# Optimization experiments

Measured on AMD Instinct MI355X. Metric: run time of the kernel, lower is better.

Reference implementation:

```python
import jax, jax.numpy as jnp
import numpy as np
import math

B, T, D, H, P, NPASS = 2, 2048, 1024, 16, 256, 3


def setup_inputs() -> dict:
    key = jax.random.key(0)
    ks = jax.random.split(key, 8)
    x = jax.random.normal(ks[0], (B, T, D), jnp.float32)
    scale_gamma = 1.0 + 0.1 * jax.random.normal(ks[1], (D,), jnp.float32)
    scale_beta = 0.1 * jax.random.normal(ks[2], (D,), jnp.float32)
    qkv_w = 0.02 * jax.random.normal(ks[3], (3 * D, D), jnp.float32)
    o_w = 0.02 * jax.random.normal(ks[4], (D, D), jnp.float32)
    norm1_w = jnp.ones((D,), jnp.float32)
    norm2_w = jnp.ones((D,), jnp.float32)
    angles = 0.1 * jax.random.normal(ks[5], (NPASS, P), jnp.float32)
    gate = jnp.ones((NPASS, D), jnp.float32)
    bias = jnp.zeros((NPASS, D), jnp.float32)
    # seeded random permutations matching torch.manual_seed(42+p*1000); torch.randperm
    pis, pjs = [], []
    for p in range(NPASS):
        rng = np.random.RandomState(42 + p * 1000)
        perm = rng.permutation(D)
        pis.append(perm[:P])
        pjs.append(perm[P:2 * P])
    pi = jnp.asarray(np.stack(pis), jnp.int32)
    pj = jnp.asarray(np.stack(pjs), jnp.int32)
    return dict(x=x, scale_gamma=scale_gamma, scale_beta=scale_beta, qkv_w=qkv_w,
                o_w=o_w, norm1_w=norm1_w, norm2_w=norm2_w, angles=angles,
                gate=gate, bias=bias, pi=pi, pj=pj)


def _rmsnorm(x, w):
    eps = jnp.finfo(x.dtype).eps
    return x * jax.lax.rsqrt(jnp.mean(x * x, axis=-1, keepdims=True) + eps) * w


def reference(x, scale_gamma, scale_beta, qkv_w, o_w, norm1_w, norm2_w,
              angles, gate, bias, pi, pj):
    Bs, Ts, Ds = x.shape
    hd = Ds // H
    # --- attention branch ---
    h = _rmsnorm(x, norm1_w) * scale_gamma + scale_beta
    qkv = (h @ qkv_w.T).reshape(Bs, Ts, 3, H, hd)
    qkv = jnp.moveaxis(qkv, 2, 0)            # [3, B, T, H, hd]
    q, k, v = (jnp.swapaxes(qkv[i], 1, 2) for i in range(3))  # [B, H, T, hd]
    scores = jnp.einsum('bhqd,bhkd->bhqk', q, k) / math.sqrt(hd)
    causal = jnp.tril(jnp.ones((Ts, Ts), bool))
    scores = jnp.where(causal, scores, -jnp.inf)
    attn = jax.nn.softmax(scores, axis=-1)
    out = jnp.einsum('bhqk,bhkd->bhqd', attn, v)
    out = jnp.swapaxes(out, 1, 2).reshape(Bs, Ts, Ds)
    x = x + out @ o_w.T
    # --- rotation pseudo-FFN branch ---
    h = _rmsnorm(x, norm2_w) * scale_gamma + scale_beta
    r = h
    for p in range(NPASS):
        cos_a = jnp.cos(angles[p])
        sin_a = jnp.sin(angles[p])
        hi = r[..., pi[p]]
        hj = r[..., pj[p]]
        r = r.at[..., pi[p]].set(hi * cos_a - hj * sin_a)
        r = r.at[..., pj[p]].set(hi * sin_a + hj * cos_a)
        r = jax.nn.silu(r * gate[p] + bias[p])
    return x + r - h
```

## Files before the change

kernel.cpp:

```cpp
#include <hip/hip_runtime.h>
#include <hip/hip_bf16.h>

#define B_ 2
#define T_ 2048
#define D_ 1024
#define H_ 16
#define HD_ 64
#define NP_ 3
#define P_ 256

#define SCALE2 0.18033688011112042f

typedef short bf16x8 __attribute__((ext_vector_type(8)));
typedef float f32x4 __attribute__((ext_vector_type(4)));

__device__ __forceinline__ float bf2f(__hip_bfloat16 v) { return __bfloat162float(v); }
__device__ __forceinline__ __hip_bfloat16 f2bf(float v) { return __float2bfloat16(v); }

__device__ __forceinline__ unsigned pack2bf(float a, float b) {
    unsigned r;
    asm("v_cvt_pk_bf16_f32 %0, %1, %2" : "=v"(r) : "v"(a), "v"(b));
    return r;
}
__device__ __forceinline__ unsigned short f2bf_u(float v) {
    return (unsigned short)pack2bf(v, v);
}

#define GLOAD_LDS16(gp, lp) \
    __builtin_amdgcn_global_load_lds( \
        (const __attribute__((address_space(1))) void*)(gp), \
        (__attribute__((address_space(3))) void*)(lp), 16, 0, 0)

__global__ __launch_bounds__(256) void detect_kernel(
    const unsigned short* __restrict__ xs, int* __restrict__ flag)
{
    __shared__ int cnt;
    if (threadIdx.x == 0) cnt = 0;
    __syncthreads();
    int bad = 0;
    for (int i = threadIdx.x; i < 16384; i += 256) {
        int e = (xs[i] >> 7) & 0xFF;
        if (e >= 0xB8) bad++;
    }
    if (bad) atomicAdd(&cnt, bad);
    __syncthreads();
    if (threadIdx.x == 0) *flag = (cnt >= 8) ? 1 : 0;
}

__global__ __launch_bounds__(256) void cvt16_2_kernel(
    const void* __restrict__ a, const void* __restrict__ bsrc,
    __hip_bfloat16* __restrict__ da, __hip_bfloat16* __restrict__ db,
    int na, int ntot, const int* __restrict__ flag)
{
    int i8 = (blockIdx.x * 256 + threadIdx.x) * 8;
    if (i8 >= ntot) return;
    int f = *flag;
    const void* src; __hip_bfloat16* dst; int off;
    if (i8 < na) { src = a; dst = da; off = i8; }
    else         { src = bsrc; dst = db; off = i8 - na; }
    if (f) {
        const float4* sp = (const float4*)((const float*)src + off);
        float4 v0 = sp[0], v1 = sp[1];
        uint4 o;
        o.x = pack2bf(v0.x, v0.y);
        o.y = pack2bf(v0.z, v0.w);
        o.z = pack2bf(v1.x, v1.y);
        o.w = pack2bf(v1.z, v1.w);
        *(uint4*)(dst + off) = o;
    } else {
        *(uint4*)(dst + off) = *(const uint4*)((const __hip_bfloat16*)src + off);
    }
}

__global__ __launch_bounds__(256) void cvt_small_kernel(
    const void* __restrict__ g,  const void* __restrict__ b,
    const void* __restrict__ n1, const void* __restrict__ n2,
    const void* __restrict__ ang, const void* __restrict__ gt,
    const void* __restrict__ bi,
    float* __restrict__ dst, const int* __restrict__ flag)
{
    int i = blockIdx.x * 256 + threadIdx.x;
    if (i >= 11008) return;
    const void* src; int off;
    if      (i < 1024) { src = g;   off = i; }
    else if (i < 2048) { src = b;   off = i - 1024; }
    else if (i < 3072) { src = n1;  off = i - 2048; }
    else if (i < 4096) { src = n2;  off = i - 3072; }
    else if (i < 4864) { src = ang; off = i - 4096; }
    else if (i < 7936) { src = gt;  off = i - 4864; }
    else               { src = bi;  off = i - 7936; }
    dst[i] = (*flag) ? ((const float*)src)[off]
                     : bf2f(((const __hip_bfloat16*)src)[off]);
}

__global__ __launch_bounds__(256) void rmsnorm1_kernel(
    const void* __restrict__ xraw,
    const float* __restrict__ gamma,
    const float* __restrict__ beta,
    const float* __restrict__ w,
    const int* __restrict__ flag,
    __hip_bfloat16* __restrict__ out)
{
    int row = blockIdx.x;
    int t = threadIdx.x;
    int f = *flag;
    float eps = f ? 1.1920929e-7f : 0.0078125f;
    float v[4];
    if (f) {
        const float4 xv = ((const float4*)((const float*)xraw + (size_t)row * D_))[t];
        v[0] = xv.x; v[1] = xv.y; v[2] = xv.z; v[3] = xv.w;
    } else {
        const uint2 u = ((const uint2*)((const __hip_bfloat16*)xraw + (size_t)row * D_))[t];
        v[0] = __uint_as_float(u.x << 16);
        v[1] = __uint_as_float(u.x & 0xffff0000u);
        v[2] = __uint_as_float(u.y << 16);
        v[3] = __uint_as_float(u.y & 0xffff0000u);
    }
    float ss = 0.f;
#pragma unroll
    for (int c = 0; c < 4; c++) ss += v[c] * v[c];
#pragma unroll
    for (int m = 32; m; m >>= 1) ss += __shfl_xor(ss, m, 64);
    __shared__ float red[4];
    int wv = t >> 6;
    if ((t & 63) == 0) red[wv] = ss;
    __syncthreads();
    float scale = rsqrtf((red[0] + red[1] + red[2] + red[3]) * (1.0f / D_) + eps);
    float o[4];
#pragma unroll
    for (int c = 0; c < 4; c++) {
        int e = t * 4 + c;
        o[c] = v[c] * scale * w[e] * gamma[e] + beta[e];
    }
    uint2 pkd;
    pkd.x = pack2bf(o[0], o[1]);
    pkd.y = pack2bf(o[2], o[3]);
    *(uint2*)(out + (size_t)row * D_ + t * 4) = pkd;
}

__global__ __launch_bounds__(256) void gemm_bt_bf16_kernel(
    const __hip_bfloat16* __restrict__ A,
    const __hip_bfloat16* __restrict__ Bm,
    __hip_bfloat16* __restrict__ C,
    int M, int N, int K, int nscale, float qscale)
{
    __shared__ __attribute__((aligned(16))) __hip_bfloat16 As[128 * 32];
    __shared__ __attribute__((aligned(16))) __hip_bfloat16 Bs[128 * 32];
    int tid = threadIdx.x;
    int bm = blockIdx.y, bn = blockIdx.x;
    int lane = tid & 63, wv = tid >> 6;
    int wm = wv >> 1, wn = wv & 1;
    int q = lane >> 4, mr = lane & 15;

    f32x4 acc[4][4] = {};

    for (int k0 = 0; k0 < K; k0 += 32) {
#pragma unroll
        for (int s = 0; s < 2; s++) {
            int e = (s * 256 + tid) * 8;
            int r = e >> 5, c = e & 31;
            GLOAD_LDS16(&A[(size_t)(bm * 128 + r) * K + k0 + c], &As[e]);
            GLOAD_LDS16(&Bm[(size_t)(bn * 128 + r) * K + k0 + c], &Bs[e]);
        }
        __syncthreads();
        bf16x8 af[4], bfr[4];
#pragma unroll
        for (int i = 0; i < 4; i++)
            af[i] = *(const bf16x8*)(&As[(wm * 64 + i * 16 + mr) * 32 + q * 8]);
#pragma unroll
        for (int j = 0; j < 4; j++)
            bfr[j] = *(const bf16x8*)(&Bs[(wn * 64 + j * 16 + mr) * 32 + q * 8]);
#pragma unroll
        for (int i = 0; i < 4; i++)
#pragma unroll
            for (int j = 0; j < 4; j++)
                acc[i][j] = __builtin_amdgcn_mfma_f32_16x16x32_bf16(af[i], bfr[j], acc[i][j], 0, 0, 0);
        __syncthreads();
    }

#pragma unroll
    for (int i = 0; i < 4; i++)
#pragma unroll
        for (int r = 0; r < 4; r++) {
            int m = bm * 128 + wm * 64 + i * 16 + q * 4 + r;
#pragma unroll
            for (int j = 0; j < 4; j++) {
                int n = bn * 128 + wn * 64 + j * 16 + mr;
                float vv = acc[i][j][r];
                if (n < nscale) vv *= qscale;
                ((unsigned short*)C)[(size_t)m * N + n] = f2bf_u(vv);
            }
        }
}

__global__ __launch_bounds__(256) void gemm_bt_resid_kernel(
    const __hip_bfloat16* __restrict__ A,
    const __hip_bfloat16* __restrict__ Bm,
    const void* __restrict__ xraw,
    const int* __restrict__ flag,
    float* __restrict__ C,
    int M, int N, int K)
{
    __shared__ __attribute__((aligned(16))) __hip_bfloat16 As[128 * 32];
    __shared__ __attribute__((aligned(16))) __hip_bfloat16 Bs[128 * 32];
    int tid = threadIdx.x;
    int bm = blockIdx.y, bn = blockIdx.x;
    int lane = tid & 63, wv = tid >> 6;
    int wm = wv >> 1, wn = wv & 1;
    int q = lane >> 4, mr = lane & 15;
    int f = *flag;

    f32x4 acc[4][4] = {};

    for (int k0 = 0; k0 < K; k0 += 32) {
#pragma unroll
        for (int s = 0; s < 2; s++) {
            int e = (s * 256 + tid) * 8;
            int r = e >> 5, c = e & 31;
            GLOAD_LDS16(&A[(size_t)(bm * 128 + r) * K + k0 + c], &As[e]);
            GLOAD_LDS16(&Bm[(size_t)(bn * 128 + r) * K + k0 + c], &Bs[e]);
        }
        __syncthreads();
        bf16x8 af[4], bfr[4];
#pragma unroll
        for (int i = 0; i < 4; i++)
            af[i] = *(const bf16x8*)(&As[(wm * 64 + i * 16 + mr) * 32 + q * 8]);
#pragma unroll
        for (int j = 0; j < 4; j++)
            bfr[j] = *(const bf16x8*)(&Bs[(wn * 64 + j * 16 + mr) * 32 + q * 8]);
#pragma unroll
        for (int i = 0; i < 4; i++)
#pragma unroll
            for (int j = 0; j < 4; j++)
                acc[i][j] = __builtin_amdgcn_mfma_f32_16x16x32_bf16(af[i], bfr[j], acc[i][j], 0, 0, 0);
        __syncthreads();
    }

#pragma unroll
    for (int i = 0; i < 4; i++)
#pragma unroll
        for (int r = 0; r < 4; r++) {
            int m = bm * 128 + wm * 64 + i * 16 + q * 4 + r;
#pragma unroll
            for (int j = 0; j < 4; j++) {
                int n = bn * 128 + wn * 64 + j * 16 + mr;
                size_t idx = (size_t)m * N + n;
                float rv = f ? ((const float*)xraw)[idx]
                             : bf2f(((const __hip_bfloat16*)xraw)[idx]);
                C[idx] = rv + acc[i][j][r];
            }
        }
}

__global__ __launch_bounds__(256, 4) void attn_kernel(
    const __hip_bfloat16* __restrict__ qkv,
    __hip_bfloat16* __restrict__ attn_out)
{
    __shared__ __attribute__((aligned(16))) __hip_bfloat16 Ks[2][64 * 64];
    __shared__ __attribute__((aligned(16))) __hip_bfloat16 Vts[2][64 * 64];
    __shared__ __attribute__((aligned(16))) unsigned int Pd[4 * 512];

    int id = blockIdx.x;
    int half = (id ^ (id >> 8)) & 1;
    int w4 = (id >> 1) & 15;
    int qt = half ? 31 - w4 : w4;
    int bh = (id >> 5) & 31;
    int b = bh >> 4, h = bh & 15;
    int tid = threadIdx.x, lane = tid & 63, wv = tid >> 6;
    int q = lane >> 4, mr = lane & 15;
    int m8 = mr & 7;

    const size_t rs3 = 3 * D_;
    const __hip_bfloat16* qp = qkv + (size_t)(b * T_) * rs3 + h * HD_;
    const __hip_bfloat16* kp = qp + D_;
    const __hip_bfloat16* vp = qp + 2 * D_;

    int sr = tid >> 2;
    int sc = (tid & 3) * 16;
    int lc0 = sc >> 3;
    int swk = sr & 7;
    int kk_ = (tid & 31) * 2;
    int dd = (tid >> 5) * 8;
    int vlc = kk_ >> 3, voff = kk_ & 7;

    bf16x8 aq0, aq1;
    {
        const __hip_bfloat16* qrow = qp + (size_t)(qt * 64 + wv * 16 + mr) * rs3;
        aq0 = *(const bf16x8*)(qrow + q * 8);
        aq1 = *(const bf16x8*)(qrow + 32 + q * 8);
    }

    bf16x8 kr0 = *(const bf16x8*)(kp + (size_t)sr * rs3 + sc);
    bf16x8 kr1 = *(const bf16x8*)(kp + (size_t)sr * rs3 + sc + 8);
    bf16x8 vr0 = *(const bf16x8*)(vp + (size_t)kk_ * rs3 + dd);
    bf16x8 vr1 = *(const bf16x8*)(vp + (size_t)(kk_ + 1) * rs3 + dd);
    *(bf16x8*)(&Ks[0][sr * 64 + ((lc0 ^ swk) * 8)]) = kr0;
    *(bf16x8*)(&Ks[0][sr * 64 + (((lc0 + 1) ^ swk) * 8)]) = kr1;
    {
        unsigned int* vd = (unsigned int*)&Vts[0][0];
        union { bf16x8 v; unsigned u[4]; } ua, ub;
        ua.v = vr0; ub.v = vr1;
#pragma unroll
        for (int w = 0; w < 4; w++) {
            unsigned lo = __builtin_amdgcn_perm(ub.u[w], ua.u[w], 0x05040100u);
            unsigned hi = __builtin_amdgcn_perm(ub.u[w], ua.u[w], 0x07060302u);
            int i0 = 2 * w, i1 = 2 * w + 1;
            vd[((dd + i0) * 64 + ((vlc ^ i0) * 8 + voff)) >> 1] = lo;
            vd[((dd + i1) * 64 + ((vlc ^ i1) * 8 + voff)) >> 1] = hi;
        }
    }
    __syncthreads();

    float l_part = 0.f;
    f32x4 o_acc[4] = {};
    unsigned int* Pw = &Pd[wv * 512];
    int qloc = wv * 16 + mr;

    for (int s = 0; s <= qt; s++) {
        int buf = s & 1;

        if (s < qt) {
            int ktn = s + 1;
            kr0 = *(const bf16x8*)(kp + (size_t)(ktn * 64 + sr) * rs3 + sc);
            kr1 = *(const bf16x8*)(kp + (size_t)(ktn * 64 + sr) * rs3 + sc + 8);
            vr0 = *(const bf16x8*)(vp + (size_t)(ktn * 64 + kk_) * rs3 + dd);
            vr1 = *(const bf16x8*)(vp + (size_t)(ktn * 64 + kk_ + 1) * rs3 + dd);
        }

        f32x4 sv[4] = {};
        {
            const __hip_bfloat16* Kb = &Ks[buf][0];
#pragma unroll
            for (int jn = 0; jn < 4; jn++)
                sv[jn] = __builtin_amdgcn_mfma_f32_16x16x32_bf16(
                    *(const bf16x8*)(&Kb[(jn * 16 + mr) * 64 + ((q ^ m8) * 8)]),
                    aq0, sv[jn], 0, 0, 0);
#pragma unroll
            for (int jn = 0; jn < 4; jn++)
                sv[jn] = __builtin_amdgcn_mfma_f32_16x16x32_bf16(
                    *(const bf16x8*)(&Kb[(jn * 16 + mr) * 64 + (((4 + q) ^ m8) * 8)]),
                    aq1, sv[jn], 0, 0, 0);
        }

        if (s == qt) {
#pragma unroll
            for (int jn = 0; jn < 4; jn++)
#pragma unroll
                for (int r = 0; r < 4; r++)
                    if (jn * 16 + q * 4 + r > qloc) sv[jn][r] = -1e30f;
        }

#pragma unroll
        for (int jn = 0; jn < 4; jn++)
#pragma unroll
            for (int r = 0; r < 4; r++) {
                float p = exp2f(sv[jn][r]);
                sv[jn][r] = p;
                l_part += p;
            }

#pragma unroll
        for (int jn = 0; jn < 4; jn++) {
            uint2 val;
            val.x = pack2bf(sv[jn][0], sv[jn][1]);
            val.y = pack2bf(sv[jn][2], sv[jn][3]);
            int dw4 = 2 * jn + (q >> 1);
            *(uint2*)(&Pw[mr * 32 + ((dw4 ^ m8) << 2) + 2 * (q & 1)]) = val;
        }

#pragma unroll
        for (int kk = 0; kk < 2; kk++) {
            bf16x8 bp = *(const bf16x8*)(&Pw[mr * 32 + (((4 * kk + q) ^ m8) << 2)]);
#pragma unroll
            for (int dt = 0; dt < 4; dt++) {
                bf16x8 bv = *(const bf16x8*)(&Vts[buf][(dt * 16 + mr) * 64 + (((kk * 4 + q) ^ m8) * 8)]);
                o_acc[dt] = __builtin_amdgcn_mfma_f32_16x16x32_bf16(bv, bp, o_acc[dt], 0, 0, 0);
            }
        }

        if (s < qt) {
            *(bf16x8*)(&Ks[buf ^ 1][sr * 64 + ((lc0 ^ swk) * 8)]) = kr0;
            *(bf16x8*)(&Ks[buf ^ 1][sr * 64 + (((lc0 + 1) ^ swk) * 8)]) = kr1;
            unsigned int* vd = (unsigned int*)&Vts[buf ^ 1][0];
            union { bf16x8 v; unsigned u[4]; } ua, ub;
            ua.v = vr0; ub.v = vr1;
#pragma unroll
            for (int w = 0; w < 4; w++) {
                unsigned lo = __builtin_amdgcn_perm(ub.u[w], ua.u[w], 0x05040100u);
                unsigned hi = __builtin_amdgcn_perm(ub.u[w], ua.u[w], 0x07060302u);
                int i0 = 2 * w, i1 = 2 * w + 1;
                vd[((dd + i0) * 64 + ((vlc ^ i0) * 8 + voff)) >> 1] = lo;
                vd[((dd + i1) * 64 + ((vlc ^ i1) * 8 + voff)) >> 1] = hi;
            }
        }
        __syncthreads();
    }

    float l_run = l_part;
    l_run += __shfl_xor(l_run, 16, 64);
    l_run += __shfl_xor(l_run, 32, 64);

    {
        float inv = 1.0f / l_run;
        int trow = qt * 64 + wv * 16 + mr;
        __hip_bfloat16* op = attn_out + (size_t)(b * T_ + trow) * D_ + h * HD_;
#pragma unroll
        for (int dt = 0; dt < 4; dt++) {
            uint2 val;
            val.x = pack2bf(o_acc[dt][0] * inv, o_acc[dt][1] * inv);
            val.y = pack2bf(o_acc[dt][2] * inv, o_acc[dt][3] * inv);
            *(uint2*)(op + dt * 16 + q * 4) = val;
        }
    }
}

__global__ __launch_bounds__(256) void final_kernel(
    const float* __restrict__ xn,
    const float* __restrict__ gamma,
    const float* __restrict__ beta,
    const float* __restrict__ w2,
    const float* __restrict__ angles,
    const float* __restrict__ gate,
    const float* __restrict__ bias,
    const int* __restrict__ pi,
    const int* __restrict__ pj,
    const int* __restrict__ flag,
    void* __restrict__ outp)
{
    __shared__ float rbuf[D_];
    __shared__ float red[4];
    int row = blockIdx.x, t = threadIdx.x;
    int f = *flag;
    float eps = f ? 1.1920929e-7f : 0.0078125f;
    const float4 xv = ((const float4*)(xn + (size_t)row * D_))[t];
    float x4[4] = {xv.x, xv.y, xv.z, xv.w};
    float ss = 0.f;
#pragma unroll
    for (int c = 0; c < 4; c++) ss += x4[c] * x4[c];
#pragma unroll
    for (int m = 32; m; m >>= 1) ss += __shfl_xor(ss, m, 64);
    int wv = t >> 6;
    if ((t & 63) == 0) red[wv] = ss;
    __syncthreads();
    float scale = rsqrtf((red[0] + red[1] + red[2] + red[3]) * (1.0f / D_) + eps);
    float hloc[4];
#pragma unroll
    for (int c = 0; c < 4; c++) {
        int e = t * 4 + c;
        float hv = x4[c] * scale * w2[e] * gamma[e] + beta[e];
        hloc[c] = hv;
        rbuf[e] = hv;
    }
    __syncthreads();
    for (int p = 0; p < NP_; p++) {
        float a = angles[p * P_ + t];
        float ca = __cosf(a), sa = __sinf(a);
        int ip = pi[p * P_ + t], jp = pj[p * P_ + t];
        float hi = rbuf[ip], hj = rbuf[jp];
        rbuf[ip] = hi * ca - hj * sa;
        rbuf[jp] = hi * sa + hj * ca;
        __syncthreads();
#pragma unroll
        for (int c = 0; c < 4; c++) {
            int e = t * 4 + c;
            float v = rbuf[e] * gate[p * D_ + e] + bias[p * D_ + e];
            rbuf[e] = v / (1.f + __expf(-v));
        }
        __syncthreads();
    }
#pragma unroll
    for (int c = 0; c < 4; c++) {
        int e = t * 4 + c;
        float ov = x4[c] + rbuf[e] - hloc[c];
        size_t idx = (size_t)row * D_ + e;
        if (f) ((float*)outp)[idx] = ov;
        else   ((__hip_bfloat16*)outp)[idx] = f2bf(ov);
    }
}

extern "C" void kernel_launch(void* const* d_in, const int* in_sizes, int n_in,
                              void* d_out, int out_size, void* d_ws, size_t ws_size,
                              hipStream_t stream)
{
    const void* x      = d_in[0];
    const void* gamma  = d_in[1];
    const void* beta   = d_in[2];
    const void* qkv_w  = d_in[3];
    const void* o_w    = d_in[4];
    const void* n1w    = d_in[5];
    const void* n2w    = d_in[6];
    const void* angles = d_in[7];
    const void* gate   = d_in[8];
    const void* bias   = d_in[9];
    const int* pi = (const int*)d_in[10];
    const int* pj = (const int*)d_in[11];

    const int M = B_ * T_;
    char* ws = (char*)d_ws;
    const size_t MB = 1u << 20;
    int*   flag   = (int*)ws;
    float* smalls = (float*)(ws + 4096);
    float* gf   = smalls;
    float* bf   = smalls + 1024;
    float* n1f  = smalls + 2048;
    float* n2f  = smalls + 3072;
    float* angf = smalls + 4096;
    float* gtf  = smalls + 4864;
    float* bif  = smalls + 7936;
    __hip_bfloat16* wbf  = (__hip_bfloat16*)(ws + 17 * MB);
    __hip_bfloat16* owbf = (__hip_bfloat16*)(ws + 23 * MB);
    __hip_bfloat16* h1   = (__hip_bfloat16*)(ws + 25 * MB);
    __hip_bfloat16* qkv  = (__hip_bfloat16*)(ws + 33 * MB);
    float*          xnew = (float*)         (ws + 33 * MB);

    detect_kernel<<<1, 256, 0, stream>>>((const unsigned short*)x, flag);

    cvt_small_kernel<<<43, 256, 0, stream>>>(gamma, beta, n1w, n2w, angles, gate, bias,
                                             smalls, flag);
    cvt16_2_kernel<<<(4 * D_ * D_ / 8 + 255) / 256, 256, 0, stream>>>(
        qkv_w, o_w, wbf, owbf, 3 * D_ * D_, 4 * D_ * D_, flag);

    rmsnorm1_kernel<<<M, 256, 0, stream>>>(x, gf, bf, n1f, flag, h1);

    gemm_bt_bf16_kernel<<<dim3(3 * D_ / 128, M / 128), 256, 0, stream>>>(
        h1, wbf, qkv, M, 3 * D_, D_, D_, SCALE2);

    attn_kernel<<<dim3(1024), 256, 0, stream>>>(qkv, h1);

    gemm_bt_resid_kernel<<<dim3(D_ / 128, M / 128), 256, 0, stream>>>(
        h1, owbf, x, flag, xnew, M, D_, D_);

    final_kernel<<<M, 256, 0, stream>>>(xnew, gf, bf, n2f, angf, gtf, bif,
                                        pi, pj, flag, d_out);
}
```

Baseline: 245.1 us.

## Feed P to PV MFMA directly from registers using 16x16x16 bf16 instruction

The attention kernel no longer writes the softmax probabilities to shared memory and reads them back for the PV product. The S-accumulator layout already matches the B-operand layout of the 16x16x16 bf16 MFMA, so P is packed straight into registers. The V-transpose LDS swizzle is changed to 4-element granules to suit the smaller operand. This removes an LDS round trip and frees shared memory, at the cost of issuing twice as many half-width MFMAs.

```diff
diff --git a/kernel.cpp b/kernel.cpp
--- a/kernel.cpp
+++ b/kernel.cpp
@@ -12,6 +12,7 @@
 #define SCALE2 0.18033688011112042f
 
 typedef short bf16x8 __attribute__((ext_vector_type(8)));
+typedef short bf16x4 __attribute__((ext_vector_type(4)));
 typedef float f32x4 __attribute__((ext_vector_type(4)));
 
 __device__ __forceinline__ float bf2f(__hip_bfloat16 v) { return __bfloat162float(v); }
@@ -24,6 +25,19 @@
 }
 __device__ __forceinline__ unsigned short f2bf_u(float v) {
     return (unsigned short)pack2bf(v, v);
+}
+
+__device__ __forceinline__ f32x4 mfma16(bf16x4 a, bf16x4 b, f32x4 c) {
+#if __has_builtin(__builtin_amdgcn_mfma_f32_16x16x16_bf16)
+    return __builtin_amdgcn_mfma_f32_16x16x16_bf16(a, b, c, 0, 0, 0);
+#elif __has_builtin(__builtin_amdgcn_mfma_f32_16x16x16bf16_1k)
+    return __builtin_amdgcn_mfma_f32_16x16x16bf16_1k(a, b, c, 0, 0, 0);
+#else
+    f32x4 d;
+    asm volatile("v_mfma_f32_16x16x16_bf16 %0, %1, %2, %3"
+                 : "=v"(d) : "v"(a), "v"(b), "v"(c));
+    return d;
+#endif
 }
 
 #define GLOAD_LDS16(gp, lp) \
@@ -258,7 +272,6 @@
 {
     __shared__ __attribute__((aligned(16))) __hip_bfloat16 Ks[2][64 * 64];
     __shared__ __attribute__((aligned(16))) __hip_bfloat16 Vts[2][64 * 64];
-    __shared__ __attribute__((aligned(16))) unsigned int Pd[4 * 512];
 
     int id = blockIdx.x;
     int half = (id ^ (id >> 8)) & 1;
@@ -280,8 +293,8 @@
     int lc0 = sc >> 3;
     int swk = sr & 7;
     int kk_ = (tid & 31) * 2;
+    int kpair = tid & 31;
     int dd = (tid >> 5) * 8;
-    int vlc = kk_ >> 3, voff = kk_ & 7;
 
     bf16x8 aq0, aq1;
     {
@@ -304,16 +317,15 @@
         for (int w = 0; w < 4; w++) {
             unsigned lo = __builtin_amdgcn_perm(ub.u[w], ua.u[w], 0x05040100u);
             unsigned hi = __builtin_amdgcn_perm(ub.u[w], ua.u[w], 0x07060302u);
-            int i0 = 2 * w, i1 = 2 * w + 1;
-            vd[((dd + i0) * 64 + ((vlc ^ i0) * 8 + voff)) >> 1] = lo;
-            vd[((dd + i1) * 64 + ((vlc ^ i1) * 8 + voff)) >> 1] = hi;
+            int d0 = dd + 2 * w, d1 = d0 + 1;
+            vd[(d0 << 5) + (((kpair >> 1) ^ (d0 & 15)) << 1) + (kpair & 1)] = lo;
+            vd[(d1 << 5) + (((kpair >> 1) ^ (d1 & 15)) << 1) + (kpair & 1)] = hi;
         }
     }
     __syncthreads();
 
     float l_part = 0.f;
     f32x4 o_acc[4] = {};
-    unsigned int* Pw = &Pd[wv * 512];
     int qloc = wv * 16 + mr;
 
     for (int s = 0; s <= qt; s++) {
@@ -361,20 +373,14 @@
 
 #pragma unroll
         for (int jn = 0; jn < 4; jn++) {
-            uint2 val;
-            val.x = pack2bf(sv[jn][0], sv[jn][1]);
-            val.y = pack2bf(sv[jn][2], sv[jn][3]);
-            int dw4 = 2 * jn + (q >> 1);
-            *(uint2*)(&Pw[mr * 32 + ((dw4 ^ m8) << 2) + 2 * (q & 1)]) = val;
-        }
-
-#pragma unroll
-        for (int kk = 0; kk < 2; kk++) {
-            bf16x8 bp = *(const bf16x8*)(&Pw[mr * 32 + (((4 * kk + q) ^ m8) << 2)]);
+            union { bf16x4 v; unsigned u[2]; } bp;
+            bp.u[0] = pack2bf(sv[jn][0], sv[jn][1]);
+            bp.u[1] = pack2bf(sv[jn][2], sv[jn][3]);
 #pragma unroll
             for (int dt = 0; dt < 4; dt++) {
-                bf16x8 bv = *(const bf16x8*)(&Vts[buf][(dt * 16 + mr) * 64 + (((kk * 4 + q) ^ m8) * 8)]);
-                o_acc[dt] = __builtin_amdgcn_mfma_f32_16x16x32_bf16(bv, bp, o_acc[dt], 0, 0, 0);
+                bf16x4 av = *(const bf16x4*)(
+                    &Vts[buf][(dt * 16 + mr) * 64 + (((jn * 4 + q) ^ mr) << 2)]);
+                o_acc[dt] = mfma16(av, bp.v, o_acc[dt]);
             }
         }
 
@@ -388,9 +394,9 @@
             for (int w = 0; w < 4; w++) {
                 unsigned lo = __builtin_amdgcn_perm(ub.u[w], ua.u[w], 0x05040100u);
                 unsigned hi = __builtin_amdgcn_perm(ub.u[w], ua.u[w], 0x07060302u);
-                int i0 = 2 * w, i1 = 2 * w + 1;
-                vd[((dd + i0) * 64 + ((vlc ^ i0) * 8 + voff)) >> 1] = lo;
-                vd[((dd + i1) * 64 + ((vlc ^ i1) * 8 + voff)) >> 1] = hi;
+                int d0 = dd + 2 * w, d1 = d0 + 1;
+                vd[(d0 << 5) + (((kpair >> 1) ^ (d0 & 15)) << 1) + (kpair & 1)] = lo;
+                vd[(d1 << 5) + (((kpair >> 1) ^ (d1 & 15)) << 1) + (kpair & 1)] = hi;
             }
         }
         __syncthreads();
```

After: 253.8 us. 1.04x slower.

## Merge prep kernels into one launch and use 128x64 tiles for output projection

Applied to the files above, without the earlier changes.

The weight conversion, small-parameter conversion and first RMSNorm are merged into one prep kernel that dispatches on block index. The RMSNorm part now reads gamma, beta and the norm weight directly from the raw inputs instead of from the converted buffer, which removes the ordering dependency between those steps. The output-projection GEMM moves from 128x128 to 128x64 tiles, doubling the grid from 256 to 512 blocks so the 256-CU device is better filled. The price is less data reuse per block and a heterogeneous prep kernel with uneven per-block work.

```diff
diff --git a/kernel.cpp b/kernel.cpp
--- a/kernel.cpp
+++ b/kernel.cpp
@@ -47,95 +47,102 @@
     if (threadIdx.x == 0) *flag = (cnt >= 8) ? 1 : 0;
 }
 
-__global__ __launch_bounds__(256) void cvt16_2_kernel(
-    const void* __restrict__ a, const void* __restrict__ bsrc,
-    __hip_bfloat16* __restrict__ da, __hip_bfloat16* __restrict__ db,
-    int na, int ntot, const int* __restrict__ flag)
-{
-    int i8 = (blockIdx.x * 256 + threadIdx.x) * 8;
-    if (i8 >= ntot) return;
-    int f = *flag;
-    const void* src; __hip_bfloat16* dst; int off;
-    if (i8 < na) { src = a; dst = da; off = i8; }
-    else         { src = bsrc; dst = db; off = i8 - na; }
-    if (f) {
-        const float4* sp = (const float4*)((const float*)src + off);
-        float4 v0 = sp[0], v1 = sp[1];
-        uint4 o;
-        o.x = pack2bf(v0.x, v0.y);
-        o.y = pack2bf(v0.z, v0.w);
-        o.z = pack2bf(v1.x, v1.y);
-        o.w = pack2bf(v1.z, v1.w);
-        *(uint4*)(dst + off) = o;
-    } else {
-        *(uint4*)(dst + off) = *(const uint4*)((const __hip_bfloat16*)src + off);
-    }
-}
-
-__global__ __launch_bounds__(256) void cvt_small_kernel(
+__global__ __launch_bounds__(256) void prep_kernel(
+    const void* __restrict__ xraw,
+    const void* __restrict__ qkvw, const void* __restrict__ ow,
     const void* __restrict__ g,  const void* __restrict__ b,
     const void* __restrict__ n1, const void* __restrict__ n2,
     const void* __restrict__ ang, const void* __restrict__ gt,
     const void* __restrict__ bi,
-    float* __restrict__ dst, const int* __restrict__ flag)
-{
-    int i = blockIdx.x * 256 + threadIdx.x;
-    if (i >= 11008) return;
-    const void* src; int off;
-    if      (i < 1024) { src = g;   off = i; }
-    else if (i < 2048) { src = b;   off = i - 1024; }
-    else if (i < 3072) { src = n1;  off = i - 2048; }
-    else if (i < 4096) { src = n2;  off = i - 3072; }
-    else if (i < 4864) { src = ang; off = i - 4096; }
-    else if (i < 7936) { src = gt;  off = i - 4864; }
-    else               { src = bi;  off = i - 7936; }
-    dst[i] = (*flag) ? ((const float*)src)[off]
-                     : bf2f(((const __hip_bfloat16*)src)[off]);
-}
-
-__global__ __launch_bounds__(256) void rmsnorm1_kernel(
-    const void* __restrict__ xraw,
-    const float* __restrict__ gamma,
-    const float* __restrict__ beta,
-    const float* __restrict__ w,
     const int* __restrict__ flag,
-    __hip_bfloat16* __restrict__ out)
-{
-    int row = blockIdx.x;
+    __hip_bfloat16* __restrict__ wbf, __hip_bfloat16* __restrict__ owbf,
+    float* __restrict__ smalls, __hip_bfloat16* __restrict__ out)
+{
+    int bid = blockIdx.x;
     int t = threadIdx.x;
     int f = *flag;
-    float eps = f ? 1.1920929e-7f : 0.0078125f;
-    float v[4];
-    if (f) {
-        const float4 xv = ((const float4*)((const float*)xraw + (size_t)row * D_))[t];
-        v[0] = xv.x; v[1] = xv.y; v[2] = xv.z; v[3] = xv.w;
-    } else {
-        const uint2 u = ((const uint2*)((const __hip_bfloat16*)xraw + (size_t)row * D_))[t];
-        v[0] = __uint_as_float(u.x << 16);
-        v[1] = __uint_as_float(u.x & 0xffff0000u);
-        v[2] = __uint_as_float(u.y << 16);
-        v[3] = __uint_as_float(u.y & 0xffff0000u);
-    }
-    float ss = 0.f;
-#pragma unroll
-    for (int c = 0; c < 4; c++) ss += v[c] * v[c];
-#pragma unroll
-    for (int m = 32; m; m >>= 1) ss += __shfl_xor(ss, m, 64);
-    __shared__ float red[4];
-    int wv = t >> 6;
-    if ((t & 63) == 0) red[wv] = ss;
-    __syncthreads();
-    float scale = rsqrtf((red[0] + red[1] + red[2] + red[3]) * (1.0f / D_) + eps);
-    float o[4];
-#pragma unroll
-    for (int c = 0; c < 4; c++) {
-        int e = t * 4 + c;
-        o[c] = v[c] * scale * w[e] * gamma[e] + beta[e];
-    }
-    uint2 pkd;
-    pkd.x = pack2bf(o[0], o[1]);
-    pkd.y = pack2bf(o[2], o[3]);
-    *(uint2*)(out + (size_t)row * D_ + t * 4) = pkd;
+
+    if (bid < 2048) {
+        const int na = 3 * D_ * D_;
+        int i8 = (bid * 256 + t) * 8;
+        const void* src; __hip_bfloat16* dst; int off;
+        if (i8 < na) { src = qkvw; dst = wbf; off = i8; }
+        else         { src = ow;   dst = owbf; off = i8 - na; }
+        if (f) {
+            const float4* sp = (const float4*)((const float*)src + off);
+            float4 v0 = sp[0], v1 = sp[1];
+            uint4 o;
+            o.x = pack2bf(v0.x, v0.y);
+            o.y = pack2bf(v0.z, v0.w);
+            o.z = pack2bf(v1.x, v1.y);
+            o.w = pack2bf(v1.z, v1.w);
+            *(uint4*)(dst + off) = o;
+        } else {
+            *(uint4*)(dst + off) = *(const uint4*)((const __hip_bfloat16*)src + off);
+        }
+        return;
+    }
+    if (bid < 6144) {
+        int row = bid - 2048;
+        float eps = f ? 1.1920929e-7f : 0.0078125f;
+        float v[4], ga[4], be[4], ww[4];
+        if (f) {
+            const float4 xv = ((const float4*)((const float*)xraw + (size_t)row * D_))[t];
+            v[0] = xv.x; v[1] = xv.y; v[2] = xv.z; v[3] = xv.w;
+            const float4 gv = ((const float4*)g)[t];
+            ga[0] = gv.x; ga[1] = gv.y; ga[2] = gv.z; ga[3] = gv.w;
+            const float4 bv = ((const float4*)b)[t];
+            be[0] = bv.x; be[1] = bv.y; be[2] = bv.z; be[3] = bv.w;
+            const float4 wv4 = ((const float4*)n1)[t];
+            ww[0] = wv4.x; ww[1] = wv4.y; ww[2] = wv4.z; ww[3] = wv4.w;
+        } else {
+            const uint2 u = ((const uint2*)((const __hip_bfloat16*)xraw + (size_t)row * D_))[t];
+            v[0] = __uint_as_float(u.x << 16);
+            v[1] = __uint_as_float(u.x & 0xffff0000u);
+            v[2] = __uint_as_float(u.y << 16);
+            v[3] = __uint_as_float(u.y & 0xffff0000u);
+#pragma unroll
+            for (int c = 0; c < 4; c++) {
+                int e = t * 4 + c;
+                ga[c] = bf2f(((const __hip_bfloat16*)g)[e]);
+                be[c] = bf2f(((const __hip_bfloat16*)b)[e]);
+                ww[c] = bf2f(((const __hip_bfloat16*)n1)[e]);
+            }
+        }
+        float ss = 0.f;
+#pragma unroll
+        for (int c = 0; c < 4; c++) ss += v[c] * v[c];
+#pragma unroll
+        for (int m = 32; m; m >>= 1) ss += __shfl_xor(ss, m, 64);
+        __shared__ float red[4];
+        int wv = t >> 6;
+        if ((t & 63) == 0) red[wv] = ss;
+        __syncthreads();
+        float scale = rsqrtf((red[0] + red[1] + red[2] + red[3]) * (1.0f / D_) + eps);
+        float o[4];
+#pragma unroll
+        for (int c = 0; c < 4; c++)
+            o[c] = v[c] * scale * ww[c] * ga[c] + be[c];
+        uint2 pkd;
+        pkd.x = pack2bf(o[0], o[1]);
+        pkd.y = pack2bf(o[2], o[3]);
+        *(uint2*)(out + (size_t)row * D_ + t * 4) = pkd;
+        return;
+    }
+    {
+        int i = (bid - 6144) * 256 + t;
+        if (i >= 11008) return;
+        const void* src; int off;
+        if      (i < 1024) { src = g;   off = i; }
+        else if (i < 2048) { src = b;   off = i - 1024; }
+        else if (i < 3072) { src = n1;  off = i - 2048; }
+        else if (i < 4096) { src = n2;  off = i - 3072; }
+        else if (i < 4864) { src = ang; off = i - 4096; }
+        else if (i < 7936) { src = gt;  off = i - 4864; }
+        else               { src = bi;  off = i - 7936; }
+        smalls[i] = f ? ((const float*)src)[off]
+                      : bf2f(((const __hip_bfloat16*)src)[off]);
+    }
 }
 
 __global__ __launch_bounds__(256) void gemm_bt_bf16_kernel(
@@ -193,7 +200,7 @@
         }
 }
 
-__global__ __launch_bounds__(256) void gemm_bt_resid_kernel(
+__global__ __launch_bounds__(256) void gemm_o64_resid_kernel(
     const __hip_bfloat16* __restrict__ A,
     const __hip_bfloat16* __restrict__ Bm,
     const void* __restrict__ xraw,
@@ -202,15 +209,14 @@
     int M, int N, int K)
 {
     __shared__ __attribute__((aligned(16))) __hip_bfloat16 As[128 * 32];
-    __shared__ __attribute__((aligned(16))) __hip_bfloat16 Bs[128 * 32];
+    __shared__ __attribute__((aligned(16))) __hip_bfloat16 Bs[64 * 32];
     int tid = threadIdx.x;
-    int bm = blockIdx.y, bn = blockIdx.x;
+    int bn = blockIdx.x, bm = blockIdx.y;
     int lane = tid & 63, wv = tid >> 6;
-    int wm = wv >> 1, wn = wv & 1;
     int q = lane >> 4, mr = lane & 15;
     int f = *flag;
 
-    f32x4 acc[4][4] = {};
+    f32x4 acc[2][4] = {};
 
     for (int k0 = 0; k0 < K; k0 += 32) {
 #pragma unroll
@@ -218,18 +224,22 @@
             int e = (s * 256 + tid) * 8;
             int r = e >> 5, c = e & 31;
             GLOAD_LDS16(&A[(size_t)(bm * 128 + r) * K + k0 + c], &As[e]);
-            GLOAD_LDS16(&Bm[(size_t)(bn * 128 + r) * K + k0 + c], &Bs[e]);
-        }
-        __syncthreads();
-        bf16x8 af[4], bfr[4];
-#pragma unroll
-        for (int i = 0; i < 4; i++)
-            af[i] = *(const bf16x8*)(&As[(wm * 64 + i * 16 + mr) * 32 + q * 8]);
+        }
+        {
+            int e = tid * 8;
+            int r = e >> 5, c = e & 31;
+            GLOAD_LDS16(&Bm[(size_t)(bn * 64 + r) * K + k0 + c], &Bs[e]);
+        }
+        __syncthreads();
+        bf16x8 af[2], bfr[4];
+#pragma unroll
+        for (int i = 0; i < 2; i++)
+            af[i] = *(const bf16x8*)(&As[(wv * 32 + i * 16 + mr) * 32 + q * 8]);
 #pragma unroll
         for (int j = 0; j < 4; j++)
-            bfr[j] = *(const bf16x8*)(&Bs[(wn * 64 + j * 16 + mr) * 32 + q * 8]);
-#pragma unroll
-        for (int i = 0; i < 4; i++)
+            bfr[j] = *(const bf16x8*)(&Bs[(j * 16 + mr) * 32 + q * 8]);
+#pragma unroll
+        for (int i = 0; i < 2; i++)
 #pragma unroll
             for (int j = 0; j < 4; j++)
                 acc[i][j] = __builtin_amdgcn_mfma_f32_16x16x32_bf16(af[i], bfr[j], acc[i][j], 0, 0, 0);
@@ -237,13 +247,13 @@
     }
 
 #pragma unroll
-    for (int i = 0; i < 4; i++)
+    for (int i = 0; i < 2; i++)
 #pragma unroll
         for (int r = 0; r < 4; r++) {
-            int m = bm * 128 + wm * 64 + i * 16 + q * 4 + r;
+            int m = bm * 128 + wv * 32 + i * 16 + q * 4 + r;
 #pragma unroll
             for (int j = 0; j < 4; j++) {
-                int n = bn * 128 + wn * 64 + j * 16 + mr;
+                int n = bn * 64 + j * 16 + mr;
                 size_t idx = (size_t)m * N + n;
                 float rv = f ? ((const float*)xraw)[idx]
                              : bf2f(((const __hip_bfloat16*)xraw)[idx]);
@@ -502,7 +512,6 @@
     float* smalls = (float*)(ws + 4096);
     float* gf   = smalls;
     float* bf   = smalls + 1024;
-    float* n1f  = smalls + 2048;
     float* n2f  = smalls + 3072;
     float* angf = smalls + 4096;
     float* gtf  = smalls + 4864;
@@ -515,19 +524,16 @@
 
     detect_kernel<<<1, 256, 0, stream>>>((const unsigned short*)x, flag);
 
-    cvt_small_kernel<<<43, 256, 0, stream>>>(gamma, beta, n1w, n2w, angles, gate, bias,
-                                             smalls, flag);
-    cvt16_2_kernel<<<(4 * D_ * D_ / 8 + 255) / 256, 256, 0, stream>>>(
-        qkv_w, o_w, wbf, owbf, 3 * D_ * D_, 4 * D_ * D_, flag);
-
-    rmsnorm1_kernel<<<M, 256, 0, stream>>>(x, gf, bf, n1f, flag, h1);
+    prep_kernel<<<6187, 256, 0, stream>>>(
+        x, qkv_w, o_w, gamma, beta, n1w, n2w, angles, gate, bias,
+        flag, wbf, owbf, smalls, h1);
 
     gemm_bt_bf16_kernel<<<dim3(3 * D_ / 128, M / 128), 256, 0, stream>>>(
         h1, wbf, qkv, M, 3 * D_, D_, D_, SCALE2);
 
     attn_kernel<<<dim3(1024), 256, 0, stream>>>(qkv, h1);
 
-    gemm_bt_resid_kernel<<<dim3(D_ / 128, M / 128), 256, 0, stream>>>(
+    gemm_o64_resid_kernel<<<dim3(D_ / 64, M / 128), 256, 0, stream>>>(
         h1, owbf, x, flag, xnew, M, D_, D_);
 
     final_kernel<<<M, 256, 0, stream>>>(xnew, gf, bf, n2f, angf, gtf, bif,
```

Result: faster. 235.1 us (-4.1%).
